# Optimization experiments

Hardware: AMD Instinct MI355X
Metric: run time of the kernel (lower is better)

## Reference

```python
import jax, jax.numpy as jnp
import numpy as np

VOXEL_SIZE = [0.4, 0.4, 0.4]
KERNEL_OFFSET = 1
MAX_NUM_NEIGHBORS = 32
PC_RANGE = [-50.0, -50.0, -5.0, 50.0, 50.0, 5.0]
N_REF, N_QUERY, N_BATCH = 500_000, 250_000, 4


def setup_inputs() -> dict:
    key = jax.random.key(0)
    k1, k2, k3, k4 = jax.random.split(key, 4)
    lo = jnp.array(PC_RANGE[:3], jnp.float32)
    hi = jnp.array(PC_RANGE[3:], jnp.float32)
    ref_xyz = jax.random.uniform(k1, (N_REF, 3), jnp.float32) * (hi - lo) + lo
    ref_b = jax.random.randint(k2, (N_REF, 1), 0, N_BATCH).astype(jnp.float32)
    q_xyz = jax.random.uniform(k3, (N_QUERY, 3), jnp.float32) * (hi - lo) + lo
    q_b = jax.random.randint(k4, (N_QUERY, 1), 0, N_BATCH).astype(jnp.float32)
    return {
        "ref_bxyz": jnp.concatenate([ref_b, ref_xyz], axis=1),
        "query_bxyz": jnp.concatenate([q_b, q_xyz], axis=1),
    }


def _ravel(vc, dims):
    # flatten (b, ix, iy, iz) voxel coords to a single int id
    return ((vc[..., 0] * dims[1] + vc[..., 1]) * dims[2] + vc[..., 2]) * dims[3] + vc[..., 3]


def reference(ref_bxyz, query_bxyz):
    ko, K = KERNEL_OFFSET, MAX_NUM_NEIGHBORS
    vsize = jnp.array([1.0 - 0.001] + VOXEL_SIZE, jnp.float32)
    pc_min = jnp.array([0.0] + PC_RANGE[:3], jnp.float32)
    pc_max = jnp.array([1.0] + PC_RANGE[3:], jnp.float32)
    pc_max = pc_max.at[0].set(ref_bxyz[:, 0].max() + 1.0)

    vc_ref = jnp.floor((ref_bxyz - pc_min) / vsize).astype(jnp.int32)   # [N,4]
    vc_q = jnp.floor((query_bxyz - pc_min) / vsize).astype(jnp.int32)   # [M,4]
    dims = jnp.ceil((pc_max - pc_min) / vsize).astype(jnp.int32) + 1    # [4]

    # 'hash table': sort ref points by flat voxel id (equivalent multimap)
    flat_ref = _ravel(vc_ref, dims)                                     # [N]
    order = jnp.argsort(flat_ref)
    svids = flat_ref[order]                                             # sorted voxel ids

    # 27 voxel offsets (qmin..qmax), batch offset = 0
    o = np.arange(-ko, ko + 1)
    offs = np.stack(np.meshgrid(o, o, o, indexing="ij"), -1).reshape(-1, 3)
    offs = np.concatenate([np.zeros((offs.shape[0], 1), np.int64), offs], 1).astype(np.int32)
    n_off = offs.shape[0]

    vc_nb = vc_q[:, None, :] + jnp.asarray(offs)[None]                  # [M,27,4]
    in_range = jnp.all((vc_nb >= 0) & (vc_nb < dims), axis=-1)          # [M,27]
    vid_nb = jnp.where(in_range, _ravel(vc_nb, dims), -1)               # [M,27]

    start = jnp.searchsorted(svids, vid_nb.reshape(-1), side="left").reshape(vid_nb.shape)
    end = jnp.searchsorted(svids, vid_nb.reshape(-1), side="right").reshape(vid_nb.shape)
    cnt = end - start                                                   # [M,27] pts per voxel
    csum = jnp.cumsum(cnt, axis=1)                                      # [M,27]
    total = csum[:, -1]                                                 # [M]

    # for each of K neighbor slots, find which window-voxel bucket it falls in
    kk = jnp.arange(K, dtype=csum.dtype)
    bucket = jax.vmap(lambda c: jnp.searchsorted(c, kk, side="right"))(csum)  # [M,K]
    csum0 = jnp.concatenate([jnp.zeros((csum.shape[0], 1), csum.dtype), csum], axis=1)
    prev = jnp.take_along_axis(csum0, bucket, axis=1)                   # edges before bucket
    pos = kk[None, :] - prev                                            # within-bucket offset
    b_cl = jnp.clip(bucket, 0, n_off - 1)
    gidx = jnp.take_along_axis(start, b_cl, axis=1) + pos               # index into sorted refs
    valid = kk[None, :] < total[:, None]                                # [M,K]
    gidx = jnp.clip(gidx, 0, svids.shape[0] - 1)

    e_ref = jnp.where(valid, order[gidx], -1)                           # [M,K] ref index or -1
    e_query = jnp.where(valid, jnp.arange(query_bxyz.shape[0], dtype=jnp.int32)[:, None], -1)

    # squared edge length (radius=1e5 in the original -> every candidate passes)
    diff = query_bxyz[:, None, 1:4] - ref_bxyz[jnp.clip(e_ref, 0), 1:4]  # [M,K,3]
    sqdist = jnp.where(valid, jnp.sum(diff * diff, axis=-1), 0.0)
    return e_ref, e_query, sqdist, valid
```

## Files before the change

kernel.cpp:

```cpp
#include <hip/hip_runtime.h>
#include <math.h>

#define NC1 251
#define NC2 251
#define NZ 26
#define D0MAX 6
#define KNB 32
#define INVX 2.5f
#define INVB (1.0f / 0.999f)
#define CAP 16
#define EMAX 8

#define NCOL (D0MAX * NC1 * NC2)
#define NCOLA 378880

__device__ __forceinline__ int vox_b(float b) { return (int)floorf(b * INVB); }
__device__ __forceinline__ int vox_x(float x) { return (int)floorf((x + 50.0f) * INVX); }
__device__ __forceinline__ int vox_z(float z) { return (int)floorf((z + 5.0f) * INVX); }
__device__ __forceinline__ int dim0_from(float bmax) {
    return (int)ceilf((bmax + 1.0f) * INVB) + 1;
}

__global__ void k_zero(uint4* __restrict__ w, int n16) {
    int i = blockIdx.x * blockDim.x + threadIdx.x;
    if (i < n16) w[i] = make_uint4(0u, 0u, 0u, 0u);
}

__global__ __launch_bounds__(256) void k_build(const float4* __restrict__ ref, int n,
                                               int* __restrict__ colcnt,
                                               unsigned* __restrict__ keyz, int* bbits) {
    __shared__ float smax[4];
    int stride = gridDim.x * blockDim.x;
    float m = 0.0f;
    for (int i = blockIdx.x * blockDim.x + threadIdx.x; i < n; i += stride) {
        float4 p = ref[i];
        m = fmaxf(m, p.x);
        int vb = vox_b(p.x), vx = vox_x(p.y), vy = vox_x(p.z), vz = vox_z(p.w);
        if (vb >= 0 && vb < D0MAX && vx >= 0 && vx < NC1 &&
            vy >= 0 && vy < NC2 && vz >= 0 && vz < NZ) {
            int col = (vb * NC1 + vx) * NC2 + vy;
            int pos = atomicAdd(&colcnt[col], 1);
            if (pos < CAP)
                keyz[col * CAP + pos] = ((unsigned)vz << 19) | (unsigned)i;
        }
    }
    for (int o = 32; o > 0; o >>= 1)
        m = fmaxf(m, __shfl_down(m, o));
    int wave = threadIdx.x >> 6;
    if ((threadIdx.x & 63) == 0) smax[wave] = m;
    __syncthreads();
    if (threadIdx.x == 0) {
        float bm = fmaxf(fmaxf(smax[0], smax[1]), fmaxf(smax[2], smax[3]));
        atomicMax(bbits, __float_as_int(bm));
    }
}

__global__ __launch_bounds__(256) void k_sortcol(const int* __restrict__ colcnt,
                                                 unsigned* __restrict__ keyz,
                                                 unsigned char* __restrict__ recs) {
    __shared__ unsigned sk[256][CAP];
    int tid = threadIdx.x;
    int col = blockIdx.x * blockDim.x + tid;
    if (col >= NCOLA) return;
    int cnt = colcnt[col];
    if (cnt > CAP) cnt = CAP;
    uint4* kb = (uint4*)(keyz + col * CAP);
    if (cnt > 0) {
        uint4 a = kb[0], b = kb[1], c = kb[2], d = kb[3];
        sk[tid][0] = a.x;  sk[tid][1] = a.y;  sk[tid][2] = a.z;  sk[tid][3] = a.w;
        sk[tid][4] = b.x;  sk[tid][5] = b.y;  sk[tid][6] = b.z;  sk[tid][7] = b.w;
        sk[tid][8] = c.x;  sk[tid][9] = c.y;  sk[tid][10] = c.z; sk[tid][11] = c.w;
        sk[tid][12] = d.x; sk[tid][13] = d.y; sk[tid][14] = d.z; sk[tid][15] = d.w;
        if (cnt > 1) {
            for (int a2 = 1; a2 < cnt; a2++) {
                unsigned key = sk[tid][a2];
                int j = a2 - 1;
                while (j >= 0 && sk[tid][j] > key) {
                    sk[tid][j + 1] = sk[tid][j];
                    j--;
                }
                sk[tid][j + 1] = key;
            }
            uint4 w0 = make_uint4(sk[tid][0], sk[tid][1], sk[tid][2], sk[tid][3]);
            uint4 w1 = make_uint4(sk[tid][4], sk[tid][5], sk[tid][6], sk[tid][7]);
            uint4 w2 = make_uint4(sk[tid][8], sk[tid][9], sk[tid][10], sk[tid][11]);
            uint4 w3 = make_uint4(sk[tid][12], sk[tid][13], sk[tid][14], sk[tid][15]);
            kb[0] = w0; kb[1] = w1; kb[2] = w2; kb[3] = w3;
        }
    }
    unsigned wrd[8];
    wrd[0] = (unsigned)(col * CAP);
#pragma unroll
    for (int i = 1; i < 8; i++) wrd[i] = 0;
    int cur = 0;
#pragma unroll
    for (int z = 0; z < 26; z++) {
        while (cur < cnt && (int)(sk[tid][cur] >> 19) <= z) cur++;
        wrd[1 + (z >> 2)] |= ((unsigned)cur) << (8 * (z & 3));
    }
    uint4* r = (uint4*)(recs + (size_t)col * 32);
    r[0] = make_uint4(wrd[0], wrd[1], wrd[2], wrd[3]);
    r[1] = make_uint4(wrd[4], wrd[5], wrd[6], wrd[7]);
}

#define WPB 4
__global__ __launch_bounds__(256) void k_query(
        const float4* __restrict__ qry, int nq,
        const unsigned char* __restrict__ recs, const unsigned* __restrict__ keyz,
        const float4* __restrict__ ref, const int* bbits,
        float* __restrict__ o_er, float* __restrict__ o_eq,
        float* __restrict__ o_sq, float* __restrict__ o_vd) {
    __shared__ int lds_i[WPB][64][EMAX + 1];
    __shared__ int lds_cnt[WPB][64];
    __shared__ float4 lds_qp[WPB][64];

    int tid = threadIdx.x;
    int wave = tid >> 6;
    int lane = tid & 63;
    int qwb = blockIdx.x * 256 + wave * 64;
    int qi = qwb + lane;
    int d0 = dim0_from(__int_as_float(*bbits));

    float4 p = make_float4(0.f, 0.f, 0.f, 0.f);
    unsigned lo[9], hi[9];
#pragma unroll
    for (int k = 0; k < 9; k++) { lo[k] = 0; hi[k] = 0; }
    bool okq = false;
    int vx = 0, vy = 0, vb = 0, zlo = 0, zhi = 2;
    if (qi < nq) {
        p = qry[qi];
        vb = vox_b(p.x);
        vx = vox_x(p.y);
        vy = vox_x(p.z);
        int vz = vox_z(p.w);
        okq = (vb >= 0 && vb < d0 && vb < D0MAX && vz >= 0 && vz < NZ);
        vb = vb < 0 ? 0 : (vb >= D0MAX ? D0MAX - 1 : vb);
        int vzc = vz < 0 ? 0 : (vz >= NZ ? NZ - 1 : vz);
        zlo = vzc - 1 > 0 ? vzc - 1 : 0;
        zhi = vzc + 2 < NZ ? vzc + 2 : NZ;
    }
    int total = 0;
    {
        int kk = 0;
#pragma unroll
        for (int ox = -1; ox <= 1; ox++) {
#pragma unroll
            for (int oy = -1; oy <= 1; oy++, kk++) {
                int nx = vx + ox, ny = vy + oy;
                bool ok = okq && nx >= 0 && nx < NC1 && ny >= 0 && ny < NC2;
                int nxc = nx < 0 ? 0 : (nx >= NC1 ? NC1 - 1 : nx);
                int nyc = ny < 0 ? 0 : (ny >= NC2 ? NC2 - 1 : ny);
                int col = (vb * NC1 + nxc) * NC2 + nyc;
                const unsigned char* r8 = recs + (size_t)col * 32;
                unsigned cs = *(const unsigned*)r8;
                unsigned plo = (zlo > 0) ? (unsigned)r8[3 + zlo] : 0u;
                unsigned phi = (unsigned)r8[3 + zhi];
                lo[kk] = ok ? cs + plo : 0u;
                hi[kk] = ok ? cs + phi : 0u;
                total += (int)(hi[kk] - lo[kk]);
            }
        }
    }
    if (total <= EMAX) {
        int emitted = 0;
#pragma unroll
        for (int k = 0; k < 9; k++)
            for (unsigned j = lo[k]; j < hi[k]; ++j)
                lds_i[wave][lane][emitted++] = (int)(keyz[j] & 0x7FFFFu);
        lds_cnt[wave][lane] = emitted;
    } else {
        lds_cnt[wave][lane] = -1;
    }
    lds_qp[wave][lane] = p;
    __syncthreads();

    size_t base = (size_t)qwb * KNB;
#pragma unroll
    for (int it = 0; it < 8; ++it) {
        int flat = (it * 64 + lane) * 4;
        int q = flat >> 5;
        int k = flat & 31;
        int qg = qwb + q;
        if (qg >= nq) continue;
        int cnt = lds_cnt[wave][q];
        if (cnt < 0) continue;
        float4 qp = lds_qp[wave][q];
        float erv[4], eqv[4], sqv[4], vdv[4];
#pragma unroll
        for (int u = 0; u < 4; ++u) {
            if (k + u < cnt) {
                int idx = lds_i[wave][q][k + u];
                float4 rp = ref[idx];
                float dx = qp.y - rp.y, dy = qp.z - rp.z, dz = qp.w - rp.w;
                erv[u] = (float)idx;
                eqv[u] = (float)qg;
                sqv[u] = dx * dx + dy * dy + dz * dz;
                vdv[u] = 1.0f;
            } else {
                erv[u] = -1.0f; eqv[u] = -1.0f; sqv[u] = 0.0f; vdv[u] = 0.0f;
            }
        }
        size_t off = base + (size_t)flat;
        *(float4*)(o_er + off) = make_float4(erv[0], erv[1], erv[2], erv[3]);
        *(float4*)(o_eq + off) = make_float4(eqv[0], eqv[1], eqv[2], eqv[3]);
        *(float4*)(o_sq + off) = make_float4(sqv[0], sqv[1], sqv[2], sqv[3]);
        *(float4*)(o_vd + off) = make_float4(vdv[0], vdv[1], vdv[2], vdv[3]);
    }

    if (qi < nq && total > EMAX) {
        size_t ro = (size_t)qi * KNB;
        int emitted = 0;
#pragma unroll
        for (int k = 0; k < 9; k++) {
            for (unsigned j = lo[k]; j < hi[k] && emitted < KNB; ++j) {
                int idx = (int)(keyz[j] & 0x7FFFFu);
                float4 rp = ref[idx];
                float dx = p.y - rp.y, dy = p.z - rp.z, dz = p.w - rp.w;
                o_er[ro + emitted] = (float)idx;
                o_eq[ro + emitted] = (float)qi;
                o_sq[ro + emitted] = dx * dx + dy * dy + dz * dz;
                o_vd[ro + emitted] = 1.0f;
                emitted++;
            }
        }
        for (int k2 = emitted; k2 < KNB; k2++) {
            o_er[ro + k2] = -1.0f;
            o_eq[ro + k2] = -1.0f;
            o_sq[ro + k2] = 0.0f;
            o_vd[ro + k2] = 0.0f;
        }
    }
}

extern "C" void kernel_launch(void* const* d_in, const int* in_sizes, int n_in,
                              void* d_out, int out_size, void* d_ws, size_t ws_size,
                              hipStream_t stream) {
    const float4* ref = (const float4*)d_in[0];
    const float4* qry = (const float4*)d_in[1];
    int n_ref = in_sizes[0] / 4;
    int n_q = in_sizes[1] / 4;
    float* out = (float*)d_out;

    size_t off_cnt = 64;
    size_t off_rec = off_cnt + (size_t)NCOLA * 4;
    size_t off_keyz = off_rec + (size_t)NCOLA * 32;
    size_t need = off_keyz + (size_t)NCOLA * CAP * 4;
    if (ws_size < need) return;

    char* w = (char*)d_ws;
    int* bbits = (int*)w;
    int* colcnt = (int*)(w + off_cnt);
    unsigned char* recs = (unsigned char*)(w + off_rec);
    unsigned* keyz = (unsigned*)(w + off_keyz);

    int n16 = (int)(off_rec / 16);
    k_zero<<<(n16 + 255) / 256, 256, 0, stream>>>((uint4*)w, n16);

    k_build<<<512, 256, 0, stream>>>(ref, n_ref, colcnt, keyz, bbits);
    k_sortcol<<<(NCOLA + 255) / 256, 256, 0, stream>>>(colcnt, keyz, recs);
    int qb = (n_q + 255) / 256;
    k_query<<<qb, 256, 0, stream>>>(qry, n_q, recs, keyz, ref, bbits,
                                    out,
                                    out + (size_t)n_q * KNB,
                                    out + 2 * (size_t)n_q * KNB,
                                    out + 3 * (size_t)n_q * KNB);
}
```

Measured before the change: 117.4 us.

## Drop per-column z-prefix records; count z-range directly from sentinel-padded sorted keys

Removes the 32-byte per-column record array that stored z-prefix counts. The sort kernel now pads empty slots with a sentinel and writes every column's sorted keys. The query kernel loads the full 64-byte key block per neighbour column and counts keys below the z bounds with comparisons. This removes the record write pass and one workspace array, but each query now reads 64 bytes instead of about 32 per column, and the sort kernel writes all columns, including empty ones.

New measurement: 127.4 us. +8.5%, slower.

```diff
diff --git a/kernel.cpp b/kernel.cpp
--- a/kernel.cpp
+++ b/kernel.cpp
@@ -10,6 +10,7 @@
 #define INVB (1.0f / 0.999f)
 #define CAP 16
 #define EMAX 8
+#define SENT 0xFFFFFFFFu
 
 #define NCOL (D0MAX * NC1 * NC2)
 #define NCOLA 378880
@@ -41,7 +42,7 @@
             int col = (vb * NC1 + vx) * NC2 + vy;
             int pos = atomicAdd(&colcnt[col], 1);
             if (pos < CAP)
-                keyz[col * CAP + pos] = ((unsigned)vz << 19) | (unsigned)i;
+                keyz[(size_t)col * CAP + pos] = ((unsigned)vz << 19) | (unsigned)i;
         }
     }
     for (int o = 32; o > 0; o >>= 1)
@@ -56,57 +57,39 @@
 }
 
 __global__ __launch_bounds__(256) void k_sortcol(const int* __restrict__ colcnt,
-                                                 unsigned* __restrict__ keyz,
-                                                 unsigned char* __restrict__ recs) {
-    __shared__ unsigned sk[256][CAP];
+                                                 unsigned* __restrict__ keyz) {
+    __shared__ unsigned sk[256][CAP + 1];
     int tid = threadIdx.x;
     int col = blockIdx.x * blockDim.x + tid;
     if (col >= NCOLA) return;
     int cnt = colcnt[col];
     if (cnt > CAP) cnt = CAP;
-    uint4* kb = (uint4*)(keyz + col * CAP);
-    if (cnt > 0) {
-        uint4 a = kb[0], b = kb[1], c = kb[2], d = kb[3];
-        sk[tid][0] = a.x;  sk[tid][1] = a.y;  sk[tid][2] = a.z;  sk[tid][3] = a.w;
-        sk[tid][4] = b.x;  sk[tid][5] = b.y;  sk[tid][6] = b.z;  sk[tid][7] = b.w;
-        sk[tid][8] = c.x;  sk[tid][9] = c.y;  sk[tid][10] = c.z; sk[tid][11] = c.w;
-        sk[tid][12] = d.x; sk[tid][13] = d.y; sk[tid][14] = d.z; sk[tid][15] = d.w;
-        if (cnt > 1) {
-            for (int a2 = 1; a2 < cnt; a2++) {
-                unsigned key = sk[tid][a2];
-                int j = a2 - 1;
-                while (j >= 0 && sk[tid][j] > key) {
-                    sk[tid][j + 1] = sk[tid][j];
-                    j--;
-                }
-                sk[tid][j + 1] = key;
-            }
-            uint4 w0 = make_uint4(sk[tid][0], sk[tid][1], sk[tid][2], sk[tid][3]);
-            uint4 w1 = make_uint4(sk[tid][4], sk[tid][5], sk[tid][6], sk[tid][7]);
-            uint4 w2 = make_uint4(sk[tid][8], sk[tid][9], sk[tid][10], sk[tid][11]);
-            uint4 w3 = make_uint4(sk[tid][12], sk[tid][13], sk[tid][14], sk[tid][15]);
-            kb[0] = w0; kb[1] = w1; kb[2] = w2; kb[3] = w3;
-        }
-    }
-    unsigned wrd[8];
-    wrd[0] = (unsigned)(col * CAP);
-#pragma unroll
-    for (int i = 1; i < 8; i++) wrd[i] = 0;
-    int cur = 0;
-#pragma unroll
-    for (int z = 0; z < 26; z++) {
-        while (cur < cnt && (int)(sk[tid][cur] >> 19) <= z) cur++;
-        wrd[1 + (z >> 2)] |= ((unsigned)cur) << (8 * (z & 3));
-    }
-    uint4* r = (uint4*)(recs + (size_t)col * 32);
-    r[0] = make_uint4(wrd[0], wrd[1], wrd[2], wrd[3]);
-    r[1] = make_uint4(wrd[4], wrd[5], wrd[6], wrd[7]);
+    uint4* kb = (uint4*)(keyz + (size_t)col * CAP);
+    uint4 a = kb[0], b = kb[1], c = kb[2], d = kb[3];
+    sk[tid][0] = a.x;  sk[tid][1] = a.y;  sk[tid][2] = a.z;  sk[tid][3] = a.w;
+    sk[tid][4] = b.x;  sk[tid][5] = b.y;  sk[tid][6] = b.z;  sk[tid][7] = b.w;
+    sk[tid][8] = c.x;  sk[tid][9] = c.y;  sk[tid][10] = c.z; sk[tid][11] = c.w;
+    sk[tid][12] = d.x; sk[tid][13] = d.y; sk[tid][14] = d.z; sk[tid][15] = d.w;
+    for (int s = cnt; s < CAP; s++) sk[tid][s] = SENT;
+    for (int a2 = 1; a2 < cnt; a2++) {
+        unsigned key = sk[tid][a2];
+        int j = a2 - 1;
+        while (j >= 0 && sk[tid][j] > key) {
+            sk[tid][j + 1] = sk[tid][j];
+            j--;
+        }
+        sk[tid][j + 1] = key;
+    }
+    kb[0] = make_uint4(sk[tid][0], sk[tid][1], sk[tid][2], sk[tid][3]);
+    kb[1] = make_uint4(sk[tid][4], sk[tid][5], sk[tid][6], sk[tid][7]);
+    kb[2] = make_uint4(sk[tid][8], sk[tid][9], sk[tid][10], sk[tid][11]);
+    kb[3] = make_uint4(sk[tid][12], sk[tid][13], sk[tid][14], sk[tid][15]);
 }
 
 #define WPB 4
 __global__ __launch_bounds__(256) void k_query(
         const float4* __restrict__ qry, int nq,
-        const unsigned char* __restrict__ recs, const unsigned* __restrict__ keyz,
+        const unsigned* __restrict__ keyz,
         const float4* __restrict__ ref, const int* bbits,
         float* __restrict__ o_er, float* __restrict__ o_eq,
         float* __restrict__ o_sq, float* __restrict__ o_vd) {
@@ -126,7 +109,8 @@
 #pragma unroll
     for (int k = 0; k < 9; k++) { lo[k] = 0; hi[k] = 0; }
     bool okq = false;
-    int vx = 0, vy = 0, vb = 0, zlo = 0, zhi = 2;
+    int vx = 0, vy = 0, vb = 0;
+    unsigned blo = 0, bhi = (unsigned)2 << 19;
     if (qi < nq) {
         p = qry[qi];
         vb = vox_b(p.x);
@@ -136,8 +120,10 @@
         okq = (vb >= 0 && vb < d0 && vb < D0MAX && vz >= 0 && vz < NZ);
         vb = vb < 0 ? 0 : (vb >= D0MAX ? D0MAX - 1 : vb);
         int vzc = vz < 0 ? 0 : (vz >= NZ ? NZ - 1 : vz);
-        zlo = vzc - 1 > 0 ? vzc - 1 : 0;
-        zhi = vzc + 2 < NZ ? vzc + 2 : NZ;
+        int zlo = vzc - 1 > 0 ? vzc - 1 : 0;
+        int zhi = vzc + 2 < NZ ? vzc + 2 : NZ;
+        blo = (unsigned)zlo << 19;
+        bhi = (unsigned)zhi << 19;
     }
     int total = 0;
     {
@@ -151,12 +137,19 @@
                 int nxc = nx < 0 ? 0 : (nx >= NC1 ? NC1 - 1 : nx);
                 int nyc = ny < 0 ? 0 : (ny >= NC2 ? NC2 - 1 : ny);
                 int col = (vb * NC1 + nxc) * NC2 + nyc;
-                const unsigned char* r8 = recs + (size_t)col * 32;
-                unsigned cs = *(const unsigned*)r8;
-                unsigned plo = (zlo > 0) ? (unsigned)r8[3 + zlo] : 0u;
-                unsigned phi = (unsigned)r8[3 + zhi];
-                lo[kk] = ok ? cs + plo : 0u;
-                hi[kk] = ok ? cs + phi : 0u;
+                const uint4* kb = (const uint4*)(keyz + (size_t)col * CAP);
+                uint4 a = kb[0], b = kb[1], c = kb[2], d = kb[3];
+                int lc = (a.x < blo) + (a.y < blo) + (a.z < blo) + (a.w < blo) +
+                         (b.x < blo) + (b.y < blo) + (b.z < blo) + (b.w < blo) +
+                         (c.x < blo) + (c.y < blo) + (c.z < blo) + (c.w < blo) +
+                         (d.x < blo) + (d.y < blo) + (d.z < blo) + (d.w < blo);
+                int hc = (a.x < bhi) + (a.y < bhi) + (a.z < bhi) + (a.w < bhi) +
+                         (b.x < bhi) + (b.y < bhi) + (b.z < bhi) + (b.w < bhi) +
+                         (c.x < bhi) + (c.y < bhi) + (c.z < bhi) + (c.w < bhi) +
+                         (d.x < bhi) + (d.y < bhi) + (d.z < bhi) + (d.w < bhi);
+                unsigned cb = (unsigned)(col * CAP);
+                lo[kk] = cb + (unsigned)lc;
+                hi[kk] = ok ? cb + (unsigned)hc : lo[kk];
                 total += (int)(hi[kk] - lo[kk]);
             }
         }
@@ -242,24 +235,22 @@
     float* out = (float*)d_out;
 
     size_t off_cnt = 64;
-    size_t off_rec = off_cnt + (size_t)NCOLA * 4;
-    size_t off_keyz = off_rec + (size_t)NCOLA * 32;
+    size_t off_keyz = off_cnt + (size_t)NCOLA * 4;
     size_t need = off_keyz + (size_t)NCOLA * CAP * 4;
     if (ws_size < need) return;
 
     char* w = (char*)d_ws;
     int* bbits = (int*)w;
     int* colcnt = (int*)(w + off_cnt);
-    unsigned char* recs = (unsigned char*)(w + off_rec);
     unsigned* keyz = (unsigned*)(w + off_keyz);
 
-    int n16 = (int)(off_rec / 16);
+    int n16 = (int)(off_keyz / 16);
     k_zero<<<(n16 + 255) / 256, 256, 0, stream>>>((uint4*)w, n16);
 
     k_build<<<512, 256, 0, stream>>>(ref, n_ref, colcnt, keyz, bbits);
-    k_sortcol<<<(NCOLA + 255) / 256, 256, 0, stream>>>(colcnt, keyz, recs);
+    k_sortcol<<<(NCOLA + 255) / 256, 256, 0, stream>>>(colcnt, keyz);
     int qb = (n_q + 255) / 256;
-    k_query<<<qb, 256, 0, stream>>>(qry, n_q, recs, keyz, ref, bbits,
+    k_query<<<qb, 256, 0, stream>>>(qry, n_q, keyz, ref, bbits,
                                     out,
                                     out + (size_t)n_q * KNB,
                                     out + 2 * (size_t)n_q * KNB,
```
